# Optimization experiments

Measured on AMD Instinct MI355X. Metric: run time of the kernel, lower is better.

Reference implementation:

```python
import math
import jax, jax.numpy as jnp
import numpy as np

NUM_BUCKETS = 32
MAX_DISTANCE = 128
N_HEADS = 16
D_KV = 64


def relative_position_bucket(rel_pos, num_buckets=NUM_BUCKETS, max_distance=MAX_DISTANCE):
    # bidirectional=True path of the original
    n = -rel_pos
    nb = num_buckets // 2
    ret = (n < 0).astype(jnp.int32) * nb
    n = jnp.abs(n)
    max_exact = nb // 2
    is_small = n < max_exact
    val_large = max_exact + (
        jnp.log(n.astype(jnp.float32) / max_exact)
        / math.log(max_distance / max_exact)
        * (nb - max_exact)
    ).astype(jnp.int32)
    val_large = jnp.minimum(val_large, nb - 1)
    return jnp.where(is_small, n, val_large) + ret


def setup_inputs() -> dict:
    key = jax.random.key(0)
    ks = jax.random.split(key, 6)
    B, S, D = 2, 2048, 1024
    inner = N_HEADS * D_KV  # 1024
    sc = 1.0 / math.sqrt(D)
    return {
        "x": jax.random.normal(ks[0], (B, S, D), dtype=jnp.float32),
        "Wq": jax.random.normal(ks[1], (D, inner), dtype=jnp.float32) * sc,
        "Wk": jax.random.normal(ks[2], (D, inner), dtype=jnp.float32) * sc,
        "Wv": jax.random.normal(ks[3], (D, inner), dtype=jnp.float32) * sc,
        "Wo": jax.random.normal(ks[4], (inner, D), dtype=jnp.float32) * sc,
        "rel_table": jax.random.normal(ks[5], (NUM_BUCKETS, N_HEADS), dtype=jnp.float32),
        "attention_mask": jnp.zeros((B, 1, 1, S), dtype=jnp.float32),
    }


def reference(x, Wq, Wk, Wv, Wo, rel_table, attention_mask):
    B, S, D = x.shape
    H, Dk = N_HEADS, D_KV

    q = (x @ Wq).reshape(B, S, H, Dk).transpose(0, 2, 1, 3)  # bhqd
    k = (x @ Wk).reshape(B, S, H, Dk).transpose(0, 2, 1, 3)
    v = (x @ Wv).reshape(B, S, H, Dk).transpose(0, 2, 1, 3)

    # NOTE: T5 attention has no 1/sqrt(d) scaling
    scores = jnp.einsum('bhqd,bhkd->bhqk', q.astype(jnp.float32), k.astype(jnp.float32))

    pos = jnp.arange(S)
    rel_pos = pos[None, :] - pos[:, None]  # [S,S] = k_pos - q_pos
    buckets = relative_position_bucket(rel_pos)
    position_bias = jnp.transpose(rel_table[buckets], (2, 0, 1))  # [H,S,S]

    scores = scores + position_bias[None, ...] + attention_mask
    weights = jax.nn.softmax(scores, axis=-1)
    out = jnp.einsum('bhqk,bhkd->bhqd', weights, v.astype(jnp.float32))
    out = out.transpose(0, 2, 1, 3).reshape(B, S, H * Dk).astype(x.dtype)
    out = out @ Wo
    return (out, position_bias)
```

## Files before the change

kernel.cpp:

```cpp
#include <hip/hip_runtime.h>
#include <hip/hip_bf16.h>
#include <math.h>
#include <stdint.h>

typedef __bf16 bf16_t;
typedef __attribute__((ext_vector_type(8))) __bf16 bf16x8;
typedef __attribute__((ext_vector_type(4))) float f32x4;
typedef unsigned short u16;
typedef unsigned int u32;

#define DEV static __device__ __forceinline__
#define LOG2E 1.4426950408889634f

DEV u16 f2b(float f){ bf16_t h = (bf16_t)f; return __builtin_bit_cast(u16, h); }
DEV float b2f(u16 u){ bf16_t h = __builtin_bit_cast(bf16_t, u); return (float)h; }
DEV f32x4 mfma16(bf16x8 a, bf16x8 b, f32x4 c){
  return __builtin_amdgcn_mfma_f32_16x16x32_bf16(a, b, c, 0, 0, 0);
}

#if __has_builtin(__builtin_amdgcn_exp2f)
DEV float fexp2(float x){ return __builtin_amdgcn_exp2f(x); }
#else
DEV float fexp2(float x){ return exp2f(x); }
#endif

DEV void gld16(const void* g, void* l){
  __builtin_amdgcn_global_load_lds((const __attribute__((address_space(1))) u32*)g,
                                   (__attribute__((address_space(3))) u32*)l, 16, 0, 0);
}

DEV bf16x8 ldsA64(const u16* arr, int row, int ch){
  return *(const bf16x8*)&arr[row*64 + ((ch ^ (row&7))*8)];
}
DEV bf16x8 ldsA32(const u16* arr, int row, int ch){
  return *(const bf16x8*)&arr[row*32 + ((ch ^ ((row>>1)&3))*8)];
}

__global__ __launch_bounds__(256) void k_convert_x(const float* __restrict__ x,
                                                   u16* __restrict__ xh, u16* __restrict__ xl){
  size_t i = ((size_t)blockIdx.x*256 + threadIdx.x)*4;
  float4 v = *(const float4*)(x + i);
  ushort4 hv, lv; float f, hf;
  f=v.x; hv.x=f2b(f); hf=b2f(hv.x); lv.x=f2b(f-hf);
  f=v.y; hv.y=f2b(f); hf=b2f(hv.y); lv.y=f2b(f-hf);
  f=v.z; hv.z=f2b(f); hf=b2f(hv.z); lv.z=f2b(f-hf);
  f=v.w; hv.w=f2b(f); hf=b2f(hv.w); lv.w=f2b(f-hf);
  *(ushort4*)(xh+i) = hv;
  *(ushort4*)(xl+i) = lv;
}

__global__ __launch_bounds__(256) void k_convert_w(const float* __restrict__ Wq, const float* __restrict__ Wk,
                                                   const float* __restrict__ Wv, const float* __restrict__ Wo,
                                                   u16* __restrict__ wth, u16* __restrict__ wtl,
                                                   u16* __restrict__ wot){
  __shared__ float tile[64][65];
  int z = blockIdx.z;
  const float* W = (z==0)?Wq:((z==1)?Wk:((z==2)?Wv:Wo));
  int n0 = blockIdx.x*64, k0 = blockIdx.y*64;
  int t = threadIdx.x;
  int r = t>>6, c = t&63;
  #pragma unroll
  for(int i=0;i<16;i++){
    int row = i*4 + r;
    tile[row][c] = W[(size_t)(k0+row)*1024 + n0 + c];
  }
  __syncthreads();
  #pragma unroll
  for(int i=0;i<16;i++){
    int nrow = i*4 + r;
    float v = tile[c][nrow];
    size_t o = (size_t)(n0+nrow)*1024 + k0 + c;
    u16 hb = f2b(v);
    if(z<3){
      wth[(size_t)z*1048576 + o] = hb;
      wtl[(size_t)z*1048576 + o] = f2b(v - b2f(hb));
    } else {
      wot[o] = hb;
    }
  }
}

__global__ __launch_bounds__(256) void k_bias_table(const float* __restrict__ rel_table,
                                                    const float* __restrict__ mask,
                                                    float* __restrict__ bt, float* __restrict__ bt2,
                                                    float* __restrict__ msk2){
  int gid = blockIdx.x*256 + threadIdx.x;
  if(gid < 4096) msk2[gid] = mask[gid]*LOG2E;
  int h = gid >> 12, idx = gid & 4095;
  float v = 0.f;
  if(idx < 4095){
    int delta = idx - 2047;
    int n = -delta;
    int ret = 0;
    if(n < 0){ ret = 16; n = -n; }
    int bucket;
    if(n < 8) bucket = n + ret;
    else {
      float a = (float)log((double)n * 0.125);
      float rr = (float)((double)a / (double)2.7725887298583984f);
      int vl = 8 + (int)(rr * 8.0f);
      vl = vl > 15 ? 15 : vl;
      bucket = vl + ret;
    }
    v = rel_table[bucket*16 + h];
  }
  bt[gid] = v;
  bt2[gid] = v*LOG2E - 32.0f;
}

__global__ __launch_bounds__(256) void k_write_bias(const float* __restrict__ bt,
                                                    float* __restrict__ out){
  size_t f = ((size_t)blockIdx.x*256 + threadIdx.x)*4;
  int h = (int)(f >> 22);
  int rem = (int)(f & 4194303);
  int q = rem >> 11;
  int k = rem & 2047;
  const float* row = bt + h*4096 + (k - q + 2047);
  float4 v = make_float4(row[0], row[1], row[2], row[3]);
  *(float4*)(out + f) = v;
}

__global__ __launch_bounds__(256) void k_gemm_qkv(const u16* __restrict__ xh, const u16* __restrict__ xl,
                                                  const u16* __restrict__ wth, const u16* __restrict__ wtl,
                                                  u16* __restrict__ qh, u16* __restrict__ ql,
                                                  u16* __restrict__ kh, u16* __restrict__ vt){
  __shared__ __align__(16) u16 SM[17408];
  u16* Ah = SM; u16* Al = SM+4096; u16* Bh = SM+8192; u16* Bl = SM+12288;
  int z = blockIdx.z;
  const u16* WH = wth + (size_t)z*1048576;
  const u16* WL = wtl + (size_t)z*1048576;
  int m0 = blockIdx.y*128, n0 = blockIdx.x*128;
  int t = threadIdx.x, w = t>>6, lane = t&63, l16 = lane&15, g = lane>>4;
  const f32x4 fzero = {0.f,0.f,0.f,0.f};
  f32x4 acc[4][4];
  #pragma unroll
  for(int i=0;i<4;i++)
    #pragma unroll
    for(int j=0;j<4;j++) acc[i][j] = fzero;
  int rbase = (w>>1)*64, cbase = (w&1)*64;
  for(int k0=0;k0<1024;k0+=32){
    __syncthreads();
    #pragma unroll
    for(int jj=0;jj<8;jj++){
      int q = w + 4*jj;
      int arr = q>>3, sub = q&7;
      if(z==2 && (arr&1)) continue;
      int row = sub*16 + (lane>>2);
      int lch = (lane&3) ^ ((row>>1)&3);
      const u16* src;
      if(arr==0)      src = xh + (size_t)(m0+row)*1024 + k0 + lch*8;
      else if(arr==1) src = xl + (size_t)(m0+row)*1024 + k0 + lch*8;
      else if(arr==2) src = WH + (size_t)(n0+row)*1024 + k0 + lch*8;
      else            src = WL + (size_t)(n0+row)*1024 + k0 + lch*8;
      gld16(src, &SM[q*512]);
    }
    __syncthreads();
    if(z==2){
      bf16x8 ah[4];
      #pragma unroll
      for(int i=0;i<4;i++) ah[i] = ldsA32(Ah, rbase + i*16 + l16, g);
      #pragma unroll
      for(int j=0;j<4;j++){
        bf16x8 bh = ldsA32(Bh, cbase + j*16 + l16, g);
        #pragma unroll
        for(int i=0;i<4;i++)
          acc[i][j] = mfma16(ah[i], bh, acc[i][j]);
      }
    } else {
      bf16x8 ah[4], am[4];
      #pragma unroll
      for(int i=0;i<4;i++){
        int row = rbase + i*16 + l16;
        ah[i] = ldsA32(Ah, row, g);
        am[i] = ldsA32(Al, row, g);
      }
      #pragma unroll
      for(int j=0;j<4;j++){
        int row = cbase + j*16 + l16;
        bf16x8 bh = ldsA32(Bh, row, g);
        bf16x8 bl = ldsA32(Bl, row, g);
        #pragma unroll
        for(int i=0;i<4;i++){
          acc[i][j] = mfma16(ah[i], bh, acc[i][j]);
          acc[i][j] = mfma16(ah[i], bl, acc[i][j]);
          acc[i][j] = mfma16(am[i], bh, acc[i][j]);
        }
      }
    }
  }
  if(z==2){
    __syncthreads();
    #pragma unroll
    for(int i=0;i<4;i++)
      #pragma unroll
      for(int j=0;j<4;j++)
        #pragma unroll
        for(int r=0;r<4;r++){
          int ml = rbase + i*16 + g*4 + r;
          int nl = cbase + j*16 + l16;
          SM[nl*136 + ml] = f2b(acc[i][j][r]);
        }
    __syncthreads();
    int bb = m0 >> 11;
    #pragma unroll
    for(int kk=0;kk<8;kk++){
      int id = t + 256*kk;
      int row = id>>4, ch = id&15;
      uint4 v = *(const uint4*)&SM[row*136 + ch*8];
      int n = n0 + row;
      size_t dst = ((size_t)(bb*16 + (n>>6))*64 + (n&63))*2048 + (m0&2047) + ch*8;
      *(uint4*)&vt[dst] = v;
    }
  } else {
    #pragma unroll
    for(int i=0;i<4;i++)
      #pragma unroll
      for(int j=0;j<4;j++)
        #pragma unroll
        for(int r=0;r<4;r++){
          int m = m0 + rbase + i*16 + g*4 + r;
          int n = n0 + cbase + j*16 + l16;
          float v = acc[i][j][r];
          if(z==0) v *= LOG2E;
          int b = m >> 11, s = m & 2047;
          int hh = n >> 6, d = n & 63;
          size_t a = ((size_t)(b*16+hh)*2048 + s)*64 + d;
          u16 hb = f2b(v);
          if(z==0){ qh[a]=hb; ql[a]=f2b(v - b2f(hb)); }
          else    { kh[a]=hb; }
        }
  }
}

__global__ __launch_bounds__(256) void k_attn(const u16* __restrict__ qh, const u16* __restrict__ ql,
                                              const u16* __restrict__ kh,
                                              const u16* __restrict__ vt, const float* __restrict__ bt2,
                                              const float* __restrict__ msk2, u16* __restrict__ ao){
  __shared__ __align__(16) u16 SM[17408];
  u16* KH = SM; u16* VT = SM+4096;
  int bh = blockIdx.y, b = bh>>4, h = bh&15;
  int q0 = blockIdx.x*128;
  int t = threadIdx.x, w = t>>6, lane = t&63, l16 = lane&15, g = lane>>4;
  size_t base  = (size_t)bh*2048*64;
  size_t vbase = (size_t)bh*64*2048;
  u16* PSw = SM + 8192 + w*2304;
  const float* bt2h = bt2 + h*4096;
  const float* msk2b = msk2 + b*2048;

  bf16x8 qfh[2][2], qfl[2][2];
  #pragma unroll
  for(int i=0;i<2;i++){
    int qr = q0 + w*32 + i*16 + l16;
    size_t a0 = base + (size_t)qr*64 + g*8;
    qfh[i][0] = *(const bf16x8*)&qh[a0];
    qfl[i][0] = *(const bf16x8*)&ql[a0];
    qfh[i][1] = *(const bf16x8*)&qh[a0+32];
    qfl[i][1] = *(const bf16x8*)&ql[a0+32];
  }
  f32x4 O[2][4];
  float rs[2][4];
  #pragma unroll
  for(int i=0;i<2;i++){
    #pragma unroll
    for(int jd=0;jd<4;jd++) O[i][jd] = {0.f,0.f,0.f,0.f};
    #pragma unroll
    for(int r=0;r<4;r++) rs[i][r] = 0.f;
  }

  for(int k0=0;k0<2048;k0+=64){
    __syncthreads();
    #pragma unroll
    for(int jj=0;jj<4;jj++){
      int q = w + 4*jj;
      int arr = q>>3, sub = q&7;
      int row = sub*8 + (lane>>3);
      int lch = (lane&7) ^ (row&7);
      const u16* src;
      if(arr==0) src = kh + base + (size_t)(k0+row)*64 + lch*8;
      else       src = vt + vbase + (size_t)row*2048 + k0 + lch*8;
      gld16(src, &SM[q*512]);
    }
    float mkj[4];
    #pragma unroll
    for(int j=0;j<4;j++) mkj[j] = msk2b[k0 + j*16 + l16];
    f32x4 sc[2][4];
    #pragma unroll
    for(int i=0;i<2;i++){
      const float* bb = bt2h + (k0 + l16 + 2047 - (q0 + w*32 + i*16 + g*4));
      #pragma unroll
      for(int j=0;j<4;j++){
        #pragma unroll
        for(int r=0;r<4;r++)
          sc[i][j][r] = bb[j*16 - r] + mkj[j];
      }
    }
    __syncthreads();
    #pragma unroll
    for(int j=0;j<4;j++){
      int krow = j*16 + l16;
      bf16x8 kfh0 = ldsA64(KH, krow, g);
      bf16x8 kfh1 = ldsA64(KH, krow, 4+g);
      #pragma unroll
      for(int i=0;i<2;i++){
        f32x4 s = sc[i][j];
        s = mfma16(qfh[i][0], kfh0, s);
        s = mfma16(qfl[i][0], kfh0, s);
        s = mfma16(qfh[i][1], kfh1, s);
        s = mfma16(qfl[i][1], kfh1, s);
        sc[i][j] = s;
      }
    }
    #pragma unroll
    for(int i=0;i<2;i++){
      #pragma unroll
      for(int j=0;j<4;j++){
        #pragma unroll
        for(int r=0;r<4;r++){
          float p = fexp2(sc[i][j][r]);
          rs[i][r] += p;
          PSw[(i*16 + g*4 + r)*72 + j*16 + l16] = f2b(p);
        }
      }
    }
    #pragma unroll
    for(int ds=0; ds<2; ds++){
      bf16x8 pa0 = *(const bf16x8*)&PSw[(     l16)*72 + ds*32 + g*8];
      bf16x8 pa1 = *(const bf16x8*)&PSw[(16 + l16)*72 + ds*32 + g*8];
      #pragma unroll
      for(int jd=0;jd<4;jd++){
        bf16x8 vb = ldsA64(VT, jd*16 + l16, ds*4 + g);
        O[0][jd] = mfma16(pa0, vb, O[0][jd]);
        O[1][jd] = mfma16(pa1, vb, O[1][jd]);
      }
    }
  }
  #pragma unroll
  for(int i=0;i<2;i++){
    float inv[4];
    #pragma unroll
    for(int r=0;r<4;r++){
      float v = rs[i][r];
      v += __shfl_xor(v,1,64);
      v += __shfl_xor(v,2,64);
      v += __shfl_xor(v,4,64);
      v += __shfl_xor(v,8,64);
      inv[r] = 1.f/v;
    }
    #pragma unroll
    for(int r=0;r<4;r++){
      int q = q0 + w*32 + i*16 + g*4 + r;
      size_t a = ((size_t)(b*2048 + q))*1024 + h*64;
      #pragma unroll
      for(int jd=0;jd<4;jd++)
        ao[a + jd*16 + l16] = f2b(O[i][jd][r]*inv[r]);
    }
  }
}

__global__ __launch_bounds__(256) void k_gemm_out(const u16* __restrict__ ao, const u16* __restrict__ wot,
                                                  float* __restrict__ out){
  __shared__ __align__(16) u16 SM[8192];
  u16* As = SM; u16* Bs = SM+4096;
  int m0 = blockIdx.y*128, n0 = blockIdx.x*128;
  int t = threadIdx.x, w = t>>6, lane = t&63, l16 = lane&15, g = lane>>4;
  f32x4 acc[4][4];
  #pragma unroll
  for(int i=0;i<4;i++)
    #pragma unroll
    for(int j=0;j<4;j++) acc[i][j] = {0.f,0.f,0.f,0.f};
  int rbase = (w>>1)*64, cbase = (w&1)*64;
  for(int k0=0;k0<1024;k0+=32){
    __syncthreads();
    #pragma unroll
    for(int jj=0;jj<4;jj++){
      int q = w + 4*jj;
      int arr = q>>3, sub = q&7;
      int row = sub*16 + (lane>>2);
      int lch = (lane&3) ^ ((row>>1)&3);
      const u16* src;
      if(arr==0) src = ao  + (size_t)(m0+row)*1024 + k0 + lch*8;
      else       src = wot + (size_t)(n0+row)*1024 + k0 + lch*8;
      gld16(src, &SM[q*512]);
    }
    __syncthreads();
    bf16x8 af[4];
    #pragma unroll
    for(int i=0;i<4;i++) af[i] = ldsA32(As, rbase + i*16 + l16, g);
    #pragma unroll
    for(int j=0;j<4;j++){
      bf16x8 bfb = ldsA32(Bs, cbase + j*16 + l16, g);
      #pragma unroll
      for(int i=0;i<4;i++)
        acc[i][j] = mfma16(af[i], bfb, acc[i][j]);
    }
  }
  #pragma unroll
  for(int i=0;i<4;i++)
    #pragma unroll
    for(int j=0;j<4;j++)
      #pragma unroll
      for(int r=0;r<4;r++){
        int m = m0 + rbase + i*16 + g*4 + r;
        int n = n0 + cbase + j*16 + l16;
        out[(size_t)m*1024 + n] = acc[i][j][r];
      }
}

extern "C" void kernel_launch(void* const* d_in, const int* in_sizes, int n_in,
                              void* d_out, int out_size, void* d_ws, size_t ws_size,
                              hipStream_t stream) {
  const float* x   = (const float*)d_in[0];
  const float* Wq  = (const float*)d_in[1];
  const float* Wk  = (const float*)d_in[2];
  const float* Wv  = (const float*)d_in[3];
  const float* Wo  = (const float*)d_in[4];
  const float* rel = (const float*)d_in[5];
  const float* msk = (const float*)d_in[6];
  float* out = (float*)d_out;
  float* bias_out = out + (size_t)4194304;
  char* ws = (char*)d_ws;
  u16* xh  = (u16*)(ws + 0);
  u16* xl  = (u16*)(ws + 8388608);
  u16* wth = (u16*)(ws + 16777216);
  u16* wtl = (u16*)(ws + 23068672);
  u16* wot = (u16*)(ws + 29360128);
  u16* qh  = (u16*)(ws + 31457280);
  u16* ql  = (u16*)(ws + 39845888);
  u16* kh  = (u16*)(ws + 48234496);
  u16* vt  = (u16*)(ws + 65011712);
  u16* ao  = (u16*)(ws + 73400320);
  float* bt   = (float*)(ws + 81788928);
  float* bt2  = (float*)(ws + 82051072);
  float* msk2 = (float*)(ws + 82313216);

  k_convert_x <<<4096, 256, 0, stream>>>(x, xh, xl);
  k_convert_w <<<dim3(16,16,4), 256, 0, stream>>>(Wq, Wk, Wv, Wo, wth, wtl, wot);
  k_bias_table<<<256, 256, 0, stream>>>(rel, msk, bt, bt2, msk2);
  k_write_bias<<<65536, 256, 0, stream>>>(bt, bias_out);
  k_gemm_qkv  <<<dim3(8,32,3), 256, 0, stream>>>(xh, xl, wth, wtl, qh, ql, kh, vt);
  k_attn      <<<dim3(16,32), 256, 0, stream>>>(qh, ql, kh, vt, bt2, msk2, ao);
  k_gemm_out  <<<dim3(8,32), 256, 0, stream>>>(ao, wot, out);
}
```

Measured before the change: 532.2 us.

## Split attention over key halves, fold mask into V and drop weight low parts

Attention now splits each (batch, head, query-tile) over two key halves, launching twice as many blocks, and writes fp32 partial outputs that a new combine kernel sums and normalises. The attention mask is folded in as exp2(mask) scaling applied to V rows, plus an extra all-ones-times-mask row in V whose MFMA column gives the softmax denominator. This removes the per-element mask add and the row-sum reductions. The low bf16 part of the QKV weights is also dropped, cutting one MFMA in three and a quarter of the global loads in the QKV GEMM. Other changes: the bias loads are vectorised, the grid is remapped, and launch bounds set occupancy hints. The costs are extra traffic for the partial outputs, one more kernel launch, and lower precision in the projections.

```diff
diff --git a/kernel.cpp b/kernel.cpp
--- a/kernel.cpp
+++ b/kernel.cpp
@@ -6,6 +6,7 @@
 typedef __bf16 bf16_t;
 typedef __attribute__((ext_vector_type(8))) __bf16 bf16x8;
 typedef __attribute__((ext_vector_type(4))) float f32x4;
+typedef float f32x4a __attribute__((ext_vector_type(4), aligned(4)));
 typedef unsigned short u16;
 typedef unsigned int u32;
 
@@ -51,8 +52,7 @@
 
 __global__ __launch_bounds__(256) void k_convert_w(const float* __restrict__ Wq, const float* __restrict__ Wk,
                                                    const float* __restrict__ Wv, const float* __restrict__ Wo,
-                                                   u16* __restrict__ wth, u16* __restrict__ wtl,
-                                                   u16* __restrict__ wot){
+                                                   u16* __restrict__ wth, u16* __restrict__ wot){
   __shared__ float tile[64][65];
   int z = blockIdx.z;
   const float* W = (z==0)?Wq:((z==1)?Wk:((z==2)?Wv:Wo));
@@ -70,22 +70,17 @@
     int nrow = i*4 + r;
     float v = tile[c][nrow];
     size_t o = (size_t)(n0+nrow)*1024 + k0 + c;
-    u16 hb = f2b(v);
-    if(z<3){
-      wth[(size_t)z*1048576 + o] = hb;
-      wtl[(size_t)z*1048576 + o] = f2b(v - b2f(hb));
-    } else {
-      wot[o] = hb;
-    }
+    if(z<3) wth[(size_t)z*1048576 + o] = f2b(v);
+    else    wot[o] = f2b(v);
   }
 }
 
 __global__ __launch_bounds__(256) void k_bias_table(const float* __restrict__ rel_table,
                                                     const float* __restrict__ mask,
                                                     float* __restrict__ bt, float* __restrict__ bt2,
-                                                    float* __restrict__ msk2){
+                                                    float* __restrict__ cf){
   int gid = blockIdx.x*256 + threadIdx.x;
-  if(gid < 4096) msk2[gid] = mask[gid]*LOG2E;
+  if(gid < 4096) cf[gid] = fexp2(mask[gid]*LOG2E);
   int h = gid >> 12, idx = gid & 4095;
   float v = 0.f;
   if(idx < 4095){
@@ -108,6 +103,12 @@
   bt2[gid] = v*LOG2E - 32.0f;
 }
 
+__global__ __launch_bounds__(256) void k_fill_crow(const float* __restrict__ cf, u16* __restrict__ vt){
+  int id = blockIdx.x*256 + threadIdx.x;
+  int bh = id >> 11, s = id & 2047, b = bh >> 4;
+  vt[(size_t)bh*133120 + 64*2048 + s] = f2b(cf[b*2048 + s]);
+}
+
 __global__ __launch_bounds__(256) void k_write_bias(const float* __restrict__ bt,
                                                     float* __restrict__ out){
   size_t f = ((size_t)blockIdx.x*256 + threadIdx.x)*4;
@@ -120,38 +121,36 @@
   *(float4*)(out + f) = v;
 }
 
-__global__ __launch_bounds__(256) void k_gemm_qkv(const u16* __restrict__ xh, const u16* __restrict__ xl,
-                                                  const u16* __restrict__ wth, const u16* __restrict__ wtl,
+__global__ __launch_bounds__(256,3) void k_gemm_qkv(const u16* __restrict__ xh, const u16* __restrict__ xl,
+                                                  const u16* __restrict__ wth, const float* __restrict__ cf,
                                                   u16* __restrict__ qh, u16* __restrict__ ql,
                                                   u16* __restrict__ kh, u16* __restrict__ vt){
   __shared__ __align__(16) u16 SM[17408];
-  u16* Ah = SM; u16* Al = SM+4096; u16* Bh = SM+8192; u16* Bl = SM+12288;
-  int z = blockIdx.z;
+  u16* Ah = SM; u16* Al = SM+4096; u16* Bh = SM+8192;
+  int z = blockIdx.y;
   const u16* WH = wth + (size_t)z*1048576;
-  const u16* WL = wtl + (size_t)z*1048576;
-  int m0 = blockIdx.y*128, n0 = blockIdx.x*128;
+  int r0 = blockIdx.x;
+  int m0 = (r0 & 31)*128, n0 = (r0 >> 5)*128;
   int t = threadIdx.x, w = t>>6, lane = t&63, l16 = lane&15, g = lane>>4;
-  const f32x4 fzero = {0.f,0.f,0.f,0.f};
   f32x4 acc[4][4];
   #pragma unroll
   for(int i=0;i<4;i++)
     #pragma unroll
-    for(int j=0;j<4;j++) acc[i][j] = fzero;
+    for(int j=0;j<4;j++) acc[i][j] = {0.f,0.f,0.f,0.f};
   int rbase = (w>>1)*64, cbase = (w&1)*64;
   for(int k0=0;k0<1024;k0+=32){
     __syncthreads();
     #pragma unroll
-    for(int jj=0;jj<8;jj++){
+    for(int jj=0;jj<6;jj++){
       int q = w + 4*jj;
       int arr = q>>3, sub = q&7;
-      if(z==2 && (arr&1)) continue;
+      if(z==2 && arr==1) continue;
       int row = sub*16 + (lane>>2);
       int lch = (lane&3) ^ ((row>>1)&3);
       const u16* src;
       if(arr==0)      src = xh + (size_t)(m0+row)*1024 + k0 + lch*8;
       else if(arr==1) src = xl + (size_t)(m0+row)*1024 + k0 + lch*8;
-      else if(arr==2) src = WH + (size_t)(n0+row)*1024 + k0 + lch*8;
-      else            src = WL + (size_t)(n0+row)*1024 + k0 + lch*8;
+      else            src = WH + (size_t)(n0+row)*1024 + k0 + lch*8;
       gld16(src, &SM[q*512]);
     }
     __syncthreads();
@@ -176,13 +175,10 @@
       }
       #pragma unroll
       for(int j=0;j<4;j++){
-        int row = cbase + j*16 + l16;
-        bf16x8 bh = ldsA32(Bh, row, g);
-        bf16x8 bl = ldsA32(Bl, row, g);
+        bf16x8 bh = ldsA32(Bh, cbase + j*16 + l16, g);
         #pragma unroll
         for(int i=0;i<4;i++){
           acc[i][j] = mfma16(ah[i], bh, acc[i][j]);
-          acc[i][j] = mfma16(ah[i], bl, acc[i][j]);
           acc[i][j] = mfma16(am[i], bh, acc[i][j]);
         }
       }
@@ -198,7 +194,8 @@
         for(int r=0;r<4;r++){
           int ml = rbase + i*16 + g*4 + r;
           int nl = cbase + j*16 + l16;
-          SM[nl*136 + ml] = f2b(acc[i][j][r]);
+          float c = cf[m0 + ml];
+          SM[nl*136 + ml] = f2b(acc[i][j][r]*c);
         }
     __syncthreads();
     int bb = m0 >> 11;
@@ -208,7 +205,7 @@
       int row = id>>4, ch = id&15;
       uint4 v = *(const uint4*)&SM[row*136 + ch*8];
       int n = n0 + row;
-      size_t dst = ((size_t)(bb*16 + (n>>6))*64 + (n&63))*2048 + (m0&2047) + ch*8;
+      size_t dst = ((size_t)(bb*16 + (n>>6))*65 + (n&63))*2048 + (m0&2047) + ch*8;
       *(uint4*)&vt[dst] = v;
     }
   } else {
@@ -232,20 +229,24 @@
   }
 }
 
-__global__ __launch_bounds__(256) void k_attn(const u16* __restrict__ qh, const u16* __restrict__ ql,
-                                              const u16* __restrict__ kh,
-                                              const u16* __restrict__ vt, const float* __restrict__ bt2,
-                                              const float* __restrict__ msk2, u16* __restrict__ ao){
-  __shared__ __align__(16) u16 SM[17408];
-  u16* KH = SM; u16* VT = SM+4096;
-  int bh = blockIdx.y, b = bh>>4, h = bh&15;
-  int q0 = blockIdx.x*128;
+__global__ __launch_bounds__(256,4) void k_attn(const u16* __restrict__ qh, const u16* __restrict__ ql,
+                                              const u16* __restrict__ kh, const u16* __restrict__ vt,
+                                              const float* __restrict__ bt2,
+                                              float* __restrict__ Op, float* __restrict__ rsp){
+  __shared__ __align__(16) u16 SM[17536];
+  u16* KH = SM; u16* VT = SM+4096; u16* C5 = SM+8192;
+  int bid = blockIdx.x;
+  int gx = bid & 7, idx = bid >> 3;
+  int bh = gx*4 + (idx & 3);
+  int idx2 = idx >> 2;
+  int q0 = (idx2 & 15)*128;
+  int kha = idx2 >> 4;
+  int b = bh >> 4, h = bh & 15;
   int t = threadIdx.x, w = t>>6, lane = t&63, l16 = lane&15, g = lane>>4;
   size_t base  = (size_t)bh*2048*64;
-  size_t vbase = (size_t)bh*64*2048;
-  u16* PSw = SM + 8192 + w*2304;
+  size_t vbase = (size_t)bh*133120;
+  u16* PSw = SM + 8320 + w*2304;
   const float* bt2h = bt2 + h*4096;
-  const float* msk2b = msk2 + b*2048;
 
   bf16x8 qfh[2][2], qfl[2][2];
   #pragma unroll
@@ -257,17 +258,14 @@
     qfh[i][1] = *(const bf16x8*)&qh[a0+32];
     qfl[i][1] = *(const bf16x8*)&ql[a0+32];
   }
-  f32x4 O[2][4];
-  float rs[2][4];
-  #pragma unroll
-  for(int i=0;i<2;i++){
-    #pragma unroll
-    for(int jd=0;jd<4;jd++) O[i][jd] = {0.f,0.f,0.f,0.f};
-    #pragma unroll
-    for(int r=0;r<4;r++) rs[i][r] = 0.f;
-  }
-
-  for(int k0=0;k0<2048;k0+=64){
+  f32x4 O[2][5];
+  #pragma unroll
+  for(int i=0;i<2;i++)
+    #pragma unroll
+    for(int jd=0;jd<5;jd++) O[i][jd] = {0.f,0.f,0.f,0.f};
+
+  int kend = kha*1024 + 1024;
+  for(int k0=kha*1024; k0<kend; k0+=64){
     __syncthreads();
     #pragma unroll
     for(int jj=0;jj<4;jj++){
@@ -280,18 +278,16 @@
       else       src = vt + vbase + (size_t)row*2048 + k0 + lch*8;
       gld16(src, &SM[q*512]);
     }
-    float mkj[4];
-    #pragma unroll
-    for(int j=0;j<4;j++) mkj[j] = msk2b[k0 + j*16 + l16];
+    if(w==0 && lane<8)
+      gld16(vt + vbase + (size_t)64*2048 + k0 + lane*8, &SM[8192]);
     f32x4 sc[2][4];
     #pragma unroll
     for(int i=0;i<2;i++){
       const float* bb = bt2h + (k0 + l16 + 2047 - (q0 + w*32 + i*16 + g*4));
       #pragma unroll
       for(int j=0;j<4;j++){
-        #pragma unroll
-        for(int r=0;r<4;r++)
-          sc[i][j][r] = bb[j*16 - r] + mkj[j];
+        f32x4a ld = *(const f32x4a*)(bb + j*16 - 3);
+        sc[i][j] = (f32x4){ld[3], ld[2], ld[1], ld[0]};
       }
     }
     __syncthreads();
@@ -311,17 +307,12 @@
       }
     }
     #pragma unroll
-    for(int i=0;i<2;i++){
-      #pragma unroll
-      for(int j=0;j<4;j++){
+    for(int i=0;i<2;i++)
+      #pragma unroll
+      for(int j=0;j<4;j++)
         #pragma unroll
-        for(int r=0;r<4;r++){
-          float p = fexp2(sc[i][j][r]);
-          rs[i][r] += p;
-          PSw[(i*16 + g*4 + r)*72 + j*16 + l16] = f2b(p);
-        }
-      }
-    }
+        for(int r=0;r<4;r++)
+          PSw[(i*16 + g*4 + r)*72 + j*16 + l16] = f2b(fexp2(sc[i][j][r]));
     #pragma unroll
     for(int ds=0; ds<2; ds++){
       bf16x8 pa0 = *(const bf16x8*)&PSw[(     l16)*72 + ds*32 + g*8];
@@ -332,29 +323,42 @@
         O[0][jd] = mfma16(pa0, vb, O[0][jd]);
         O[1][jd] = mfma16(pa1, vb, O[1][jd]);
       }
-    }
-  }
+      bf16x8 vb5 = *(const bf16x8*)&C5[ds*32 + g*8];
+      O[0][4] = mfma16(pa0, vb5, O[0][4]);
+      O[1][4] = mfma16(pa1, vb5, O[1][4]);
+    }
+  }
+  size_t pbase = ((size_t)kha*32 + bh)*2048;
   #pragma unroll
   for(int i=0;i<2;i++){
-    float inv[4];
-    #pragma unroll
-    for(int r=0;r<4;r++){
-      float v = rs[i][r];
-      v += __shfl_xor(v,1,64);
-      v += __shfl_xor(v,2,64);
-      v += __shfl_xor(v,4,64);
-      v += __shfl_xor(v,8,64);
-      inv[r] = 1.f/v;
-    }
     #pragma unroll
     for(int r=0;r<4;r++){
       int q = q0 + w*32 + i*16 + g*4 + r;
-      size_t a = ((size_t)(b*2048 + q))*1024 + h*64;
+      size_t oo = (pbase + q)*64;
       #pragma unroll
       for(int jd=0;jd<4;jd++)
-        ao[a + jd*16 + l16] = f2b(O[i][jd][r]*inv[r]);
-    }
-  }
+        Op[oo + jd*16 + l16] = O[i][jd][r];
+      if(l16==0) rsp[pbase + q] = O[i][4][r];
+    }
+  }
+}
+
+__global__ __launch_bounds__(256) void k_combine(const float* __restrict__ Op, const float* __restrict__ rsp,
+                                                 u16* __restrict__ ao){
+  size_t fid = ((size_t)blockIdx.x*256 + threadIdx.x)*4;
+  int m = (int)(fid >> 10), n = (int)(fid & 1023);
+  int bh = (m>>11)*16 + (n>>6);
+  int q = m & 2047, d = n & 63;
+  size_t po = ((size_t)bh*2048 + q)*64 + d;
+  f32x4 a = *(const f32x4*)&Op[po];
+  f32x4 c = *(const f32x4*)&Op[po + 4194304];
+  float inv = 1.f/(rsp[bh*2048 + q] + rsp[bh*2048 + q + 65536]);
+  ushort4 o;
+  o.x = f2b((a[0]+c[0])*inv);
+  o.y = f2b((a[1]+c[1])*inv);
+  o.z = f2b((a[2]+c[2])*inv);
+  o.w = f2b((a[3]+c[3])*inv);
+  *(ushort4*)&ao[fid] = o;
 }
 
 __global__ __launch_bounds__(256) void k_gemm_out(const u16* __restrict__ ao, const u16* __restrict__ wot,
@@ -422,22 +426,25 @@
   u16* xh  = (u16*)(ws + 0);
   u16* xl  = (u16*)(ws + 8388608);
   u16* wth = (u16*)(ws + 16777216);
-  u16* wtl = (u16*)(ws + 23068672);
-  u16* wot = (u16*)(ws + 29360128);
-  u16* qh  = (u16*)(ws + 31457280);
-  u16* ql  = (u16*)(ws + 39845888);
-  u16* kh  = (u16*)(ws + 48234496);
-  u16* vt  = (u16*)(ws + 65011712);
-  u16* ao  = (u16*)(ws + 73400320);
-  float* bt   = (float*)(ws + 81788928);
-  float* bt2  = (float*)(ws + 82051072);
-  float* msk2 = (float*)(ws + 82313216);
+  u16* wot = (u16*)(ws + 23068672);
+  u16* qh  = (u16*)(ws + 25165824);
+  u16* ql  = (u16*)(ws + 33554432);
+  u16* kh  = (u16*)(ws + 41943040);
+  u16* vt  = (u16*)(ws + 50331648);
+  u16* ao  = (u16*)(ws + 58982400);
+  float* Op  = (float*)(ws + 67371008);
+  float* rsp = (float*)(ws + 100925440);
+  float* bt  = (float*)(ws + 101449728);
+  float* bt2 = (float*)(ws + 101711872);
+  float* cf  = (float*)(ws + 101974016);
 
   k_convert_x <<<4096, 256, 0, stream>>>(x, xh, xl);
-  k_convert_w <<<dim3(16,16,4), 256, 0, stream>>>(Wq, Wk, Wv, Wo, wth, wtl, wot);
-  k_bias_table<<<256, 256, 0, stream>>>(rel, msk, bt, bt2, msk2);
+  k_convert_w <<<dim3(16,16,4), 256, 0, stream>>>(Wq, Wk, Wv, Wo, wth, wot);
+  k_bias_table<<<256, 256, 0, stream>>>(rel, msk, bt, bt2, cf);
+  k_fill_crow <<<256, 256, 0, stream>>>(cf, vt);
   k_write_bias<<<65536, 256, 0, stream>>>(bt, bias_out);
-  k_gemm_qkv  <<<dim3(8,32,3), 256, 0, stream>>>(xh, xl, wth, wtl, qh, ql, kh, vt);
-  k_attn      <<<dim3(16,32), 256, 0, stream>>>(qh, ql, kh, vt, bt2, msk2, ao);
+  k_gemm_qkv  <<<dim3(256,3), 256, 0, stream>>>(xh, xl, wth, cf, qh, ql, kh, vt);
+  k_attn      <<<1024, 256, 0, stream>>>(qh, ql, kh, vt, bt2, Op, rsp);
+  k_combine   <<<4096, 256, 0, stream>>>(Op, rsp, ao);
   k_gemm_out  <<<dim3(8,32), 256, 0, stream>>>(ao, wot, out);
 }
```

New measurement: 637.2 us. 1.2x slower.
